# Kernel tuning notes

Measured on AMD Instinct MI355X. Metric: run time of the kernel, lower is better.

The kernel has to match this reference:

```python
import jax, jax.numpy as jnp
import numpy as np
from jax import lax

EPS_NORM = 1e-12   # F.normalize default eps
KS = 3             # fixed 3x3 window
K2 = KS * KS
MIN_CONN, MAX_CONN = 1, 8
NUM_GROUPS = 16    # largest divisor <=16 of C=128
GN_EPS = 1e-5


def _unfold3x3_reflect(x):
    # x: [B,C,H,W] -> patches [B,C,9,H,W] (reflect-padded 3x3 neighborhoods)
    B, C, H, W = x.shape
    p = jnp.pad(x, ((0, 0), (0, 0), (1, 1), (1, 1)), mode='reflect')
    pats = [p[:, :, dy:dy + H, dx:dx + W] for dy in range(KS) for dx in range(KS)]
    return jnp.stack(pats, axis=2)


def _df_counts(x):
    # DFDetector: mean over C, fixed Laplacian conv (zero pad), abs, per-batch min-max norm
    B = x.shape[0]
    avg = jnp.mean(x, axis=1, keepdims=True)  # [B,1,H,W]
    kern = jnp.array([[0., -1., 0.], [-1., 4., -1.], [0., -1., 0.]],
                     dtype=x.dtype).reshape(1, 1, 3, 3)
    df = jnp.abs(lax.conv_general_dilated(
        avg, kern, window_strides=(1, 1), padding=((1, 1), (1, 1)),
        dimension_numbers=('NCHW', 'OIHW', 'NCHW')))
    dmin = df.reshape(B, -1).min(axis=1).reshape(B, 1, 1, 1)
    dmax = df.reshape(B, -1).max(axis=1).reshape(B, 1, 1, 1)
    dn = (df - dmin) / (dmax - dmin + 1e-8)
    return MIN_CONN + jnp.round(dn * (MAX_CONN - MIN_CONN))  # [B,1,H,W], values in [1,8]


def _group_norm(x, w, b):
    B, C, H, W = x.shape
    g = x.reshape(B, NUM_GROUPS, -1)
    mu = g.mean(-1, keepdims=True)
    var = g.var(-1, keepdims=True)  # biased, matches torch GroupNorm
    g = (g - mu) * lax.rsqrt(var + GN_EPS)
    return g.reshape(B, C, H, W) * w[None, :, None, None] + b[None, :, None, None]


def setup_inputs() -> dict:
    key = jax.random.key(0)
    ks = jax.random.split(key, 7)
    B, C, H, W = 8, 128, 96, 96
    return {
        'x': jax.random.normal(ks[0], (B, C, H, W), jnp.float32),
        'gn_weight': jax.random.uniform(ks[1], (C,), jnp.float32, 0.5, 1.5),
        'gn_bias': jax.random.normal(ks[2], (C,), jnp.float32) * 0.1,
        'w1': jax.random.normal(ks[3], (2 * C, C), jnp.float32) * 0.02,
        'b1': jax.random.normal(ks[4], (2 * C,), jnp.float32) * 0.02,
        'w2': jax.random.normal(ks[5], (C, 2 * C), jnp.float32) * 0.02,
        'b2': jax.random.normal(ks[6], (C,), jnp.float32) * 0.02,
    }


def reference(x, gn_weight, gn_bias, w1, b1, w2, b2):
    B, C, H, W = x.shape
    P = H * W
    # per-pixel connection counts (integer k in [1,8]); non-differentiable in original
    counts = lax.stop_gradient(_df_counts(x))
    kvals = jnp.minimum(counts, K2).astype(jnp.int32).reshape(B, 1, P)

    patches = _unfold3x3_reflect(x).reshape(B, C, K2, P)
    xc = x.reshape(B, C, P)
    # L2 normalize over channel dim (F.normalize, eps=1e-12)
    cn = xc / jnp.maximum(jnp.linalg.norm(xc, axis=1, keepdims=True), EPS_NORM)
    pn = patches / jnp.maximum(jnp.linalg.norm(patches, axis=1, keepdims=True), EPS_NORM)

    sim = jnp.einsum('bcp,bckp->bkp', cn, pn)          # [B,9,P] cosine sims
    order = jnp.argsort(-sim, axis=1)                   # descending (== topk order)
    top_sim = jnp.take_along_axis(sim, order, axis=1)
    mask = jnp.arange(K2)[None, :, None] < kvals        # rank < k -> selected
    wts = jnp.exp(top_sim) * mask
    wts = wts / jnp.sum(wts, axis=1, keepdims=True)     # softmax over selected sims

    pat_sorted = jnp.take_along_axis(patches, order[:, None, :, :], axis=2)
    out = jnp.einsum('bckp,bkp->bcp', pat_sorted, wts).reshape(B, C, H, W)

    enhanced = out + _group_norm(x, gn_weight, gn_bias)
    h = jax.nn.relu(jnp.einsum('oi,bihw->bohw', w1, enhanced) + b1[None, :, None, None])
    ffn = jnp.einsum('oi,bihw->bohw', w2, h) + b2[None, :, None, None]
    return enhanced + ffn
```

## Files before the change

### kernel.cpp

```cpp
#include <hip/hip_runtime.h>

#define BD 8
#define CD 128
#define HD 96
#define WD 96
#define PD 9216
#define ND 73728

typedef __attribute__((ext_vector_type(8))) short short8;
typedef __attribute__((ext_vector_type(4))) float f32x4;

__device__ inline float bfu2f(unsigned int u) { return __uint_as_float(u << 16); }
__device__ inline unsigned short f2bfu(float f) {
  unsigned int u = __float_as_uint(f);
  u += 0x7fffu + ((u >> 16) & 1u);
  return (unsigned short)(u >> 16);
}

template<bool F32>
__device__ __forceinline__ float ldv(const void* __restrict__ p, size_t i) {
  if constexpr (F32) return ((const float*)p)[i];
  else return bfu2f(((const unsigned short*)p)[i]);
}

__global__ void k_init(unsigned long long* dmm, int* cnt) {
  int t = threadIdx.x;
  if (t < 8) dmm[t] = 0x7FEFFFFFFFFFFFFFULL;
  else if (t < 16) dmm[t] = 0ULL;
  if (t == 16) { cnt[0] = 0; cnt[1] = 0; }
}

__global__ void k_detect(const unsigned int* __restrict__ xw, int* __restrict__ cnt) {
  int t = blockIdx.x * 256 + threadIdx.x;
  uint4 w = ((const uint4*)xw)[t];
  int lz = (int)((w.x & 0xFFFFu) == 0u) + (int)((w.y & 0xFFFFu) == 0u) +
           (int)((w.z & 0xFFFFu) == 0u) + (int)((w.w & 0xFFFFu) == 0u);
  int e2 = (int)(((w.x >> 7) & 0xFFu) == 0xFFu) + (int)(((w.y >> 7) & 0xFFu) == 0xFFu) +
           (int)(((w.z >> 7) & 0xFFu) == 0xFFu) + (int)(((w.w >> 7) & 0xFFu) == 0xFFu);
  #pragma unroll
  for (int off = 32; off; off >>= 1) {
    lz += __shfl_down(lz, off);
    e2 += __shfl_down(e2, off);
  }
  if ((threadIdx.x & 63) == 0) { atomicAdd(&cnt[0], lz); atomicAdd(&cnt[1], e2); }
}

__global__ void k_flag(const int* __restrict__ cnt, int* __restrict__ flag) {
  *flag = (cnt[0] > 4096 || cnt[1] > 0) ? 1 : 0;
}

__global__ void k_cvtw(const void* __restrict__ w1, const void* __restrict__ w2,
                       unsigned short* __restrict__ wc, const int* __restrict__ flag) {
  bool f32 = (*flag != 0);
  int t = blockIdx.x * 256 + threadIdx.x;
  if (t < 32768)
    wc[t] = f32 ? f2bfu(((const float*)w1)[t]) : ((const unsigned short*)w1)[t];
  else {
    int u = t - 32768;
    wc[t] = f32 ? f2bfu(((const float*)w2)[u]) : ((const unsigned short*)w2)[u];
  }
}

__global__ void k_cvtb(const void* __restrict__ gw, const void* __restrict__ gb,
                       const void* __restrict__ b1, const void* __restrict__ b2,
                       float* __restrict__ prm, const int* __restrict__ flag) {
  bool f32 = (*flag != 0);
  int t = threadIdx.x;
  for (int i = t; i < 640; i += 256) {
    float v;
    if (i < 128)      v = f32 ? ((const float*)gw)[i]       : bfu2f(((const unsigned short*)gw)[i]);
    else if (i < 256) v = f32 ? ((const float*)gb)[i - 128] : bfu2f(((const unsigned short*)gb)[i - 128]);
    else if (i < 512) v = f32 ? ((const float*)b1)[i - 256] : bfu2f(((const unsigned short*)b1)[i - 256]);
    else              v = f32 ? ((const float*)b2)[i - 512] : bfu2f(((const unsigned short*)b2)[i - 512]);
    prm[i] = v;
  }
}

template<bool F32>
__device__ __forceinline__ void pmt_body(const void* __restrict__ x,
                                         float* __restrict__ xpm,
                                         double* __restrict__ avg, double* __restrict__ nrm,
                                         double* __restrict__ nrm2,
                                         double* __restrict__ gpart,
                                         float (*tile)[132], int lb) {
  const int t = threadIdx.x, px = t & 63, ci = t >> 6;
  const int gp0 = lb * 64, b = gp0 / PD, p0 = gp0 - b * PD;
  double sg[4] = {0.0, 0.0, 0.0, 0.0}, qg[4] = {0.0, 0.0, 0.0, 0.0};
  for (int j = 0; j < 32; ++j) {
    int c = ci * 32 + j;
    float v = ldv<F32>(x, (size_t)(b * CD + c) * PD + p0 + px);
    tile[px][c] = v;
    sg[j >> 3] += (double)v;
    qg[j >> 3] += (double)v * (double)v;
  }
  #pragma unroll
  for (int g = 0; g < 4; ++g) {
    #pragma unroll
    for (int off = 32; off; off >>= 1) {
      sg[g] += __shfl_down(sg[g], off);
      qg[g] += __shfl_down(qg[g], off);
    }
  }
  if (px == 0) {
    double* gp_ = gpart + (size_t)lb * 32;
    #pragma unroll
    for (int g = 0; g < 4; ++g) {
      gp_[(ci * 4 + g) * 2 + 0] = sg[g];
      gp_[(ci * 4 + g) * 2 + 1] = qg[g];
    }
  }
  __syncthreads();
  for (int i = t; i < 2048; i += 256) {
    int r = i >> 5, seg = i & 31;
    *(float4*)(xpm + (size_t)(gp0 + r) * 128 + seg * 4) = *(const float4*)&tile[r][seg * 4];
  }
  if (t < 64) {
    double s = 0.0, q = 0.0;
    for (int c = 0; c < 128; ++c) {
      float v = tile[t][c];
      s += (double)v;
      q += (double)v * (double)v;
    }
    double qq[4] = {0.0, 0.0, 0.0, 0.0};
    #pragma unroll
    for (int g = 0; g < 4; ++g)
      for (int i = 0; i < 32; ++i) {
        float v = tile[t][g * 32 + i];
        qq[g] += (double)v * (double)v;
      }
    avg[gp0 + t] = s * (1.0 / 128.0);
    nrm[gp0 + t] = sqrt(q);
    nrm2[gp0 + t] = ((qq[0] + qq[1]) + qq[2]) + qq[3];
  }
}
__global__ __launch_bounds__(256) void k_pmt(const void* __restrict__ x,
                                             const int* __restrict__ flag,
                                             float* __restrict__ xpm,
                                             double* __restrict__ avg,
                                             double* __restrict__ nrm,
                                             double* __restrict__ nrm2,
                                             double* __restrict__ gpart) {
  __shared__ float tile[64][132];
  const int lb = (blockIdx.x & 7) * 144 + (blockIdx.x >> 3);
  if (*flag) pmt_body<true>(x, xpm, avg, nrm, nrm2, gpart, tile, lb);
  else pmt_body<false>(x, xpm, avg, nrm, nrm2, gpart, tile, lb);
}

__global__ void k_gn2(const double* __restrict__ gpart, float* __restrict__ gn) {
  const int bg = blockIdx.x;
  const int b = bg >> 4, g = bg & 15;
  const int t = threadIdx.x;
  double s = 0.0, q = 0.0;
  for (int i = t; i < 144; i += 64) {
    const double* pp = gpart + (size_t)(b * 144 + i) * 32 + g * 2;
    s += pp[0];
    q += pp[1];
  }
  #pragma unroll
  for (int off = 32; off; off >>= 1) {
    s += __shfl_down(s, off);
    q += __shfl_down(q, off);
  }
  if (t == 0) {
    double mu = s / 73728.0;
    double var = q / 73728.0 - mu * mu;
    gn[bg] = (float)mu;
    gn[128 + bg] = (float)(1.0 / sqrt(var + 1e-5));
  }
}

__device__ inline double lap_df(const double* __restrict__ a, int b, int y, int x) {
  const double* ab = a + (size_t)b * PD;
  double v = 4.0 * ab[y * WD + x];
  if (y > 0)      v -= ab[(y - 1) * WD + x];
  if (y < HD - 1) v -= ab[(y + 1) * WD + x];
  if (x > 0)      v -= ab[y * WD + x - 1];
  if (x < WD - 1) v -= ab[y * WD + x + 1];
  return fabs(v);
}

__global__ void k_minmax(const double* __restrict__ avg, unsigned long long* __restrict__ dmm,
                         double* __restrict__ dfb) {
  __shared__ double mnW[4], mxW[4];
  int t = threadIdx.x;
  const int lb = (blockIdx.x & 7) * 36 + (blockIdx.x >> 3);
  int gp = lb * 256 + t;
  int b = gp / PD, p = gp - b * PD;
  double df = lap_df(avg, b, p / WD, p % WD);
  dfb[gp] = df;
  double mn = df, mx = df;
  #pragma unroll
  for (int off = 32; off; off >>= 1) {
    mn = fmin(mn, __shfl_down(mn, off));
    mx = fmax(mx, __shfl_down(mx, off));
  }
  if ((t & 63) == 0) { mnW[t >> 6] = mn; mxW[t >> 6] = mx; }
  __syncthreads();
  if (t == 0) {
    mn = fmin(fmin(mnW[0], mnW[1]), fmin(mnW[2], mnW[3]));
    mx = fmax(fmax(mxW[0], mxW[1]), fmax(mxW[2], mxW[3]));
    atomicMin(&dmm[b], (unsigned long long)__double_as_longlong(mn));
    atomicMax(&dmm[b + 8], (unsigned long long)__double_as_longlong(mx));
  }
}

__global__ __launch_bounds__(256, 3) void k_ipg(const float* __restrict__ xpm,
                                                const double* __restrict__ nrm,
                                                const double* __restrict__ nrm2,
                                                const double* __restrict__ dfb,
                                                const unsigned long long* __restrict__ dmm,
                                                const float* __restrict__ gn,
                                                const float* __restrict__ prm,
                                                unsigned short* __restrict__ eg) {
  __shared__ float tileF[12800];
  __shared__ double nsl[100];
  __shared__ double nsl2[64];
  float4* tile4 = (float4*)tileF;
  const float* gwf = prm;
  const float* gbf = prm + 128;

  const int t = threadIdx.x;
  const int lb = (blockIdx.x & 7) * 144 + (blockIdx.x >> 3);
  const int b = lb / 144;
  const int tid = lb - b * 144;
  const int ty = tid / 12, tx = tid - ty * 12;
  const int y0 = ty * 8, x0 = tx * 8;

  {
    const int s = t & 31, hpb = t >> 5;
    #pragma unroll
    for (int it = 0; it < 13; ++it) {
      int hp = it * 8 + hpb;
      if (hp < 100) {
        int hr = hp / 10, hc = hp - hr * 10;
        int gy = y0 - 1 + hr; gy = gy < 0 ? -gy : (gy >= HD ? 2 * HD - 2 - gy : gy);
        int gx = x0 - 1 + hc; gx = gx < 0 ? -gx : (gx >= WD ? 2 * WD - 2 - gx : gx);
        const float4* src = (const float4*)(xpm + (size_t)(b * PD + gy * WD + gx) * 128) + s;
        tile4[(hp * 32 + s) ^ (hp & 7)] = *src;
      }
    }
    if (t < 100) {
      int hr = t / 10, hc = t - hr * 10;
      int gy = y0 - 1 + hr; gy = gy < 0 ? -gy : (gy >= HD ? 2 * HD - 2 - gy : gy);
      int gx = x0 - 1 + hc; gx = gx < 0 ? -gx : (gx >= WD ? 2 * WD - 2 - gx : gx);
      nsl[t] = nrm[b * PD + gy * WD + gx];
    } else if (t >= 128 && t < 192) {
      int a2 = t - 128;
      nsl2[a2] = nrm2[b * PD + (y0 + (a2 >> 3)) * WD + x0 + (a2 & 7)];
    }
  }
  __syncthreads();

  const int a = t >> 2, q = t & 3;
  const int yl = a >> 3, xl = a & 7;
  const int y = y0 + yl, xx = x0 + xl;
  const int p = y * WD + xx;
  const int cpix = (yl + 1) * 10 + (xl + 1);
  const int cub = cpix * 32 + q * 8, csw = cpix & 7;

  double sd[9];
  {
    float cv[32];
    #pragma unroll
    for (int j4 = 0; j4 < 8; ++j4)
      *(float4*)(cv + 4 * j4) = tile4[(cub + j4) ^ csw];
    #pragma unroll
    for (int k = 0; k < 9; ++k) {
      if (k == 4) continue;
      int dy = k / 3, dx = k - dy * 3;
      int pix = (yl + dy) * 10 + (xl + dx);
      int ub = pix * 32 + q * 8, sw = pix & 7;
      double acc = 0.0;
      #pragma unroll
      for (int seg = 0; seg < 8; ++seg) {
        float4 nv = tile4[(ub + seg) ^ sw];
        acc += (double)cv[seg * 4 + 0] * (double)nv.x;
        acc += (double)cv[seg * 4 + 1] * (double)nv.y;
        acc += (double)cv[seg * 4 + 2] * (double)nv.z;
        acc += (double)cv[seg * 4 + 3] * (double)nv.w;
      }
      double v1 = __shfl_down(acc, 1);
      double v2 = __shfl_down(acc, 2);
      double v3 = __shfl_down(acc, 3);
      sd[k] = ((acc + v1) + v2) + v3;
    }
  }

  float wv[9];
  #pragma unroll
  for (int j = 0; j < 9; ++j) wv[j] = 0.f;
  if (q == 0) {
    double dmin = __longlong_as_double((long long)dmm[b]);
    double dmax = __longlong_as_double((long long)dmm[b + 8]);
    double df = dfb[b * PD + p];
    double dn = (df - dmin) / (dmax - dmin + 1e-8);
    int kk = 1 + (int)rint(dn * 7.0);
    kk = kk < 1 ? 1 : (kk > 8 ? 8 : kk);

    sd[4] = nsl2[a];
    double np_ = fmax(nsl[cpix], 1e-12);
    #pragma unroll
    for (int k = 0; k < 9; ++k) {
      int dy = k / 3, dx = k - dy * 3;
      double nq = fmax(nsl[(yl + dy) * 10 + (xl + dx)], 1e-12);
      sd[k] = sd[k] / (np_ * nq);
    }
    float w[9];
    float wsum = 0.f;
    #pragma unroll
    for (int j = 0; j < 9; ++j) {
      int rank = 0;
      #pragma unroll
      for (int i = 0; i < 9; ++i)
        rank += (sd[i] > sd[j]) || (sd[i] == sd[j] && i < j);
      w[j] = (rank < kk) ? expf((float)sd[j]) : 0.f;
      wsum += w[j];
    }
    float inv = 1.f / wsum;
    #pragma unroll
    for (int j = 0; j < 9; ++j) wv[j] = w[j] * inv;
  }
  #pragma unroll
  for (int j = 0; j < 9; ++j) wv[j] = __shfl(wv[j], (t & 63) & ~3);

  {
    float og[32];
    #pragma unroll
    for (int j = 0; j < 32; ++j) og[j] = 0.f;
    #pragma unroll
    for (int k = 0; k < 9; ++k) {
      int dy = k / 3, dx = k - dy * 3;
      int pix = (yl + dy) * 10 + (xl + dx);
      int ub = pix * 32 + q * 8, sw = pix & 7;
      #pragma unroll
      for (int seg = 0; seg < 8; ++seg) {
        float4 nv = tile4[(ub + seg) ^ sw];
        og[seg * 4 + 0] += wv[k] * nv.x;
        og[seg * 4 + 1] += wv[k] * nv.y;
        og[seg * 4 + 2] += wv[k] * nv.z;
        og[seg * 4 + 3] += wv[k] * nv.w;
      }
    }
    const int g16 = b * 16;
    unsigned short* egr = eg + (size_t)(b * PD + p) * 128 + q * 32;
    #pragma unroll
    for (int seg = 0; seg < 4; ++seg) {
      float4 cA = tile4[(cub + seg * 2) ^ csw];
      float4 cB = tile4[(cub + seg * 2 + 1) ^ csw];
      float cvv[8] = {cA.x, cA.y, cA.z, cA.w, cB.x, cB.y, cB.z, cB.w};
      int g = q * 4 + seg;
      float mu = gn[g16 + g], rs = gn[128 + g16 + g];
      unsigned int pkd[4];
      #pragma unroll
      for (int j = 0; j < 8; ++j) {
        int c = q * 32 + seg * 8 + j;
        float e = og[seg * 8 + j] + (cvv[j] - mu) * rs * gwf[c] + gbf[c];
        unsigned int h = (unsigned int)f2bfu(e);
        if (j & 1) pkd[j >> 1] |= h << 16;
        else pkd[j >> 1] = h;
      }
      uint4 v; v.x = pkd[0]; v.y = pkd[1]; v.z = pkd[2]; v.w = pkd[3];
      *(uint4*)(egr + seg * 8) = v;
    }
  }
}

__global__ __launch_bounds__(256, 3) void k_ffn(const unsigned short* __restrict__ eg,
                                                const float* __restrict__ prm,
                                                const unsigned short* __restrict__ wc,
                                                float* __restrict__ outp) {
  __shared__ unsigned short et[64][136];
  __shared__ unsigned short Hl[64][264];
  const float* b1f = prm + 256;
  const float* b2f = prm + 512;

  const int t = threadIdx.x;
  const int lb = (blockIdx.x & 7) * 144 + (blockIdx.x >> 3);
  const int gp0 = lb * 64;
  const int b = gp0 / PD, p0b = gp0 - b * PD;

  const unsigned short* wc1 = wc;
  const unsigned short* wc2 = wc + 32768;
  const int lane = t & 63, wave = t >> 6;
  const int r16 = lane & 15, quad = lane >> 4;

  {
    const uint4* eg4 = (const uint4*)(eg + (size_t)gp0 * 128);
    #pragma unroll
    for (int it = 0; it < 4; ++it) {
      int lin = it * 256 + t;
      int row = lin >> 4, c8 = lin & 15;
      *(uint4*)&et[row][c8 * 8] = eg4[lin];
    }
  }
  short8 wb1[16];
  #pragma unroll
  for (int kk = 0; kk < 4; ++kk)
    #pragma unroll
    for (int nt = 0; nt < 4; ++nt)
      wb1[kk * 4 + nt] = *(const short8*)(wc1 + (size_t)(wave * 64 + nt * 16 + r16) * 128 + kk * 32 + quad * 8);
  __syncthreads();

  f32x4 acc[16];
  #pragma unroll
  for (int i = 0; i < 16; ++i) acc[i] = (f32x4){0.f, 0.f, 0.f, 0.f};
  #pragma unroll
  for (int kk = 0; kk < 4; ++kk) {
    short8 afm[4];
    #pragma unroll
    for (int m = 0; m < 4; ++m)
      afm[m] = *(const short8*)&et[m * 16 + r16][kk * 32 + quad * 8];
    #pragma unroll
    for (int nt = 0; nt < 4; ++nt)
      #pragma unroll
      for (int m = 0; m < 4; ++m)
        acc[m * 4 + nt] = __builtin_amdgcn_mfma_f32_16x16x32_bf16(afm[m], wb1[kk * 4 + nt], acc[m * 4 + nt], 0, 0, 0);
  }
  #pragma unroll
  for (int nt = 0; nt < 4; ++nt) {
    int n = wave * 64 + nt * 16 + r16;
    float bias = b1f[n];
    #pragma unroll
    for (int m = 0; m < 4; ++m)
      #pragma unroll
      for (int r = 0; r < 4; ++r)
        Hl[m * 16 + quad * 4 + r][n] = f2bfu(fmaxf(acc[m * 4 + nt][r] + bias, 0.f));
  }
  short8 wb2[16];
  #pragma unroll
  for (int kk = 0; kk < 8; ++kk)
    #pragma unroll
    for (int nt = 0; nt < 2; ++nt)
      wb2[kk * 2 + nt] = *(const short8*)(wc2 + (size_t)(wave * 32 + nt * 16 + r16) * 256 + kk * 32 + quad * 8);
  __syncthreads();

  f32x4 acc2[8];
  #pragma unroll
  for (int i = 0; i < 8; ++i) acc2[i] = (f32x4){0.f, 0.f, 0.f, 0.f};
  #pragma unroll
  for (int kk = 0; kk < 8; ++kk) {
    short8 afm[4];
    #pragma unroll
    for (int m = 0; m < 4; ++m)
      afm[m] = *(const short8*)&Hl[m * 16 + r16][kk * 32 + quad * 8];
    #pragma unroll
    for (int nt = 0; nt < 2; ++nt)
      #pragma unroll
      for (int m = 0; m < 4; ++m)
        acc2[m * 2 + nt] = __builtin_amdgcn_mfma_f32_16x16x32_bf16(afm[m], wb2[kk * 2 + nt], acc2[m * 2 + nt], 0, 0, 0);
  }
  #pragma unroll
  for (int nt = 0; nt < 2; ++nt) {
    int n = wave * 32 + nt * 16 + r16;
    float bias = b2f[n];
    #pragma unroll
    for (int m = 0; m < 4; ++m) {
      int mloc0 = m * 16 + quad * 4;
      float4 o;
      o.x = acc2[m * 2 + nt][0] + bias + bfu2f(et[mloc0 + 0][n]);
      o.y = acc2[m * 2 + nt][1] + bias + bfu2f(et[mloc0 + 1][n]);
      o.z = acc2[m * 2 + nt][2] + bias + bfu2f(et[mloc0 + 2][n]);
      o.w = acc2[m * 2 + nt][3] + bias + bfu2f(et[mloc0 + 3][n]);
      *(float4*)(outp + (size_t)(b * CD + n) * PD + p0b + mloc0) = o;
    }
  }
}

extern "C" void kernel_launch(void* const* d_in, const int* in_sizes, int n_in,
                              void* d_out, int out_size, void* d_ws, size_t ws_size,
                              hipStream_t stream) {
  const void* x  = d_in[0];
  const void* gw = d_in[1];
  const void* gb = d_in[2];
  const void* w1 = d_in[3];
  const void* b1 = d_in[4];
  const void* w2 = d_in[5];
  const void* b2 = d_in[6];
  float* out = (float*)d_out;

  char* ws = (char*)d_ws;
  int* flag = (int*)ws;
  int* cnt = (int*)(ws + 16);
  unsigned long long* dmm = (unsigned long long*)(ws + 128);
  float* gn = (float*)(ws + 256);
  float* prm = (float*)(ws + 1280);
  unsigned short* wc = (unsigned short*)(ws + 3840);
  double* avg = (double*)(ws + 134912);
  double* nrm = (double*)(ws + 724736);
  double* nrm2 = (double*)(ws + 1314560);
  double* gpart = (double*)(ws + 1904384);
  double* dfb = (double*)(ws + 2199296);
  unsigned short* eg = (unsigned short*)(ws + 2789120);
  float* xpm = (float*)(ws + 21663488);

  k_init<<<1, 64, 0, stream>>>(dmm, cnt);
  k_detect<<<64, 256, 0, stream>>>((const unsigned int*)x, cnt);
  k_flag<<<1, 1, 0, stream>>>(cnt, flag);
  k_cvtw<<<256, 256, 0, stream>>>(w1, w2, wc, flag);
  k_cvtb<<<1, 256, 0, stream>>>(gw, gb, b1, b2, prm, flag);
  k_pmt<<<ND / 64, 256, 0, stream>>>(x, flag, xpm, avg, nrm, nrm2, gpart);
  k_gn2<<<128, 64, 0, stream>>>(gpart, gn);
  k_minmax<<<ND / 256, 256, 0, stream>>>(avg, dmm, dfb);
  k_ipg<<<ND / 64, 256, 0, stream>>>(xpm, nrm, nrm2, dfb, dmm, gn, prm, eg);
  k_ffn<<<ND / 64, 256, 0, stream>>>(eg, prm, wc, out);
}
```

Baseline: 188.3 us.

## Drop pixel-major transpose buffer and merge small setup kernels

The stats pass no longer writes a transposed pixel-major copy of x. It reads x directly in NCHW with coalesced per-pixel threads and computes the norms and group partial sums in registers. The gather kernel now loads the halo tile straight from the NCHW input with strided per-channel loads. The init, flag, weight and bias conversion kernels are fused into one launch, and group-norm finalisation is merged with the Laplacian min/max kernel, cutting the launch count from ten to six. This removes a full write and reread of the transposed activation copy, but the gather's scalar strided loads from x may be less efficient than the earlier float4 row reads.

```diff
diff --git a/kernel.cpp b/kernel.cpp
--- a/kernel.cpp
+++ b/kernel.cpp
@@ -23,16 +23,10 @@
   else return bfu2f(((const unsigned short*)p)[i]);
 }
 
-__global__ void k_init(unsigned long long* dmm, int* cnt) {
-  int t = threadIdx.x;
-  if (t < 8) dmm[t] = 0x7FEFFFFFFFFFFFFFULL;
-  else if (t < 16) dmm[t] = 0ULL;
-  if (t == 16) { cnt[0] = 0; cnt[1] = 0; }
-}
-
-__global__ void k_detect(const unsigned int* __restrict__ xw, int* __restrict__ cnt) {
-  int t = blockIdx.x * 256 + threadIdx.x;
-  uint4 w = ((const uint4*)xw)[t];
+__global__ void k_detect(const unsigned int* __restrict__ xw, int* __restrict__ dcnt) {
+  __shared__ int wl[4], we[4];
+  const int t = threadIdx.x;
+  uint4 w = ((const uint4*)xw)[blockIdx.x * 256 + t];
   int lz = (int)((w.x & 0xFFFFu) == 0u) + (int)((w.y & 0xFFFFu) == 0u) +
            (int)((w.z & 0xFFFFu) == 0u) + (int)((w.w & 0xFFFFu) == 0u);
   int e2 = (int)(((w.x >> 7) & 0xFFu) == 0xFFu) + (int)(((w.y >> 7) & 0xFFu) == 0xFFu) +
@@ -42,131 +36,105 @@
     lz += __shfl_down(lz, off);
     e2 += __shfl_down(e2, off);
   }
-  if ((threadIdx.x & 63) == 0) { atomicAdd(&cnt[0], lz); atomicAdd(&cnt[1], e2); }
-}
-
-__global__ void k_flag(const int* __restrict__ cnt, int* __restrict__ flag) {
-  *flag = (cnt[0] > 4096 || cnt[1] > 0) ? 1 : 0;
-}
-
-__global__ void k_cvtw(const void* __restrict__ w1, const void* __restrict__ w2,
-                       unsigned short* __restrict__ wc, const int* __restrict__ flag) {
-  bool f32 = (*flag != 0);
-  int t = blockIdx.x * 256 + threadIdx.x;
-  if (t < 32768)
-    wc[t] = f32 ? f2bfu(((const float*)w1)[t]) : ((const unsigned short*)w1)[t];
-  else {
-    int u = t - 32768;
-    wc[t] = f32 ? f2bfu(((const float*)w2)[u]) : ((const unsigned short*)w2)[u];
-  }
-}
-
-__global__ void k_cvtb(const void* __restrict__ gw, const void* __restrict__ gb,
-                       const void* __restrict__ b1, const void* __restrict__ b2,
-                       float* __restrict__ prm, const int* __restrict__ flag) {
-  bool f32 = (*flag != 0);
-  int t = threadIdx.x;
-  for (int i = t; i < 640; i += 256) {
-    float v;
-    if (i < 128)      v = f32 ? ((const float*)gw)[i]       : bfu2f(((const unsigned short*)gw)[i]);
-    else if (i < 256) v = f32 ? ((const float*)gb)[i - 128] : bfu2f(((const unsigned short*)gb)[i - 128]);
-    else if (i < 512) v = f32 ? ((const float*)b1)[i - 256] : bfu2f(((const unsigned short*)b1)[i - 256]);
-    else              v = f32 ? ((const float*)b2)[i - 512] : bfu2f(((const unsigned short*)b2)[i - 512]);
-    prm[i] = v;
+  if ((t & 63) == 0) { wl[t >> 6] = lz; we[t >> 6] = e2; }
+  __syncthreads();
+  if (t == 0) {
+    dcnt[blockIdx.x] = wl[0] + wl[1] + wl[2] + wl[3];
+    dcnt[64 + blockIdx.x] = we[0] + we[1] + we[2] + we[3];
+  }
+}
+
+__global__ void k_cvt(const void* __restrict__ w1, const void* __restrict__ w2,
+                      const void* __restrict__ gw, const void* __restrict__ gb,
+                      const void* __restrict__ b1, const void* __restrict__ b2,
+                      const int* __restrict__ dcnt,
+                      unsigned short* __restrict__ wc, float* __restrict__ prm,
+                      int* __restrict__ flag, unsigned long long* __restrict__ dmm) {
+  __shared__ int sflag;
+  const int t = threadIdx.x;
+  if (t < 64) {
+    int lz = dcnt[t], e2 = dcnt[64 + t];
+    #pragma unroll
+    for (int off = 32; off; off >>= 1) {
+      lz += __shfl_down(lz, off);
+      e2 += __shfl_down(e2, off);
+    }
+    if (t == 0) sflag = (lz > 4096 || e2 > 0) ? 1 : 0;
+  }
+  __syncthreads();
+  const bool f32 = sflag != 0;
+  const int blk = blockIdx.x;
+  if (blk < 256) {
+    int i = blk * 256 + t;
+    if (i < 32768)
+      wc[i] = f32 ? f2bfu(((const float*)w1)[i]) : ((const unsigned short*)w1)[i];
+    else {
+      int u = i - 32768;
+      wc[i] = f32 ? f2bfu(((const float*)w2)[u]) : ((const unsigned short*)w2)[u];
+    }
+  } else {
+    for (int i = t; i < 640; i += 256) {
+      float v;
+      if (i < 128)      v = f32 ? ((const float*)gw)[i]       : bfu2f(((const unsigned short*)gw)[i]);
+      else if (i < 256) v = f32 ? ((const float*)gb)[i - 128] : bfu2f(((const unsigned short*)gb)[i - 128]);
+      else if (i < 512) v = f32 ? ((const float*)b1)[i - 256] : bfu2f(((const unsigned short*)b1)[i - 256]);
+      else              v = f32 ? ((const float*)b2)[i - 512] : bfu2f(((const unsigned short*)b2)[i - 512]);
+      prm[i] = v;
+    }
+    if (t < 8) dmm[t] = 0x7FEFFFFFFFFFFFFFULL;
+    else if (t < 16) dmm[t - 8 + 8] = 0ULL;
+    if (t == 16) *flag = sflag;
   }
 }
 
 template<bool F32>
-__device__ __forceinline__ void pmt_body(const void* __restrict__ x,
-                                         float* __restrict__ xpm,
-                                         double* __restrict__ avg, double* __restrict__ nrm,
-                                         double* __restrict__ nrm2,
-                                         double* __restrict__ gpart,
-                                         float (*tile)[132], int lb) {
-  const int t = threadIdx.x, px = t & 63, ci = t >> 6;
-  const int gp0 = lb * 64, b = gp0 / PD, p0 = gp0 - b * PD;
-  double sg[4] = {0.0, 0.0, 0.0, 0.0}, qg[4] = {0.0, 0.0, 0.0, 0.0};
-  for (int j = 0; j < 32; ++j) {
-    int c = ci * 32 + j;
-    float v = ldv<F32>(x, (size_t)(b * CD + c) * PD + p0 + px);
-    tile[px][c] = v;
-    sg[j >> 3] += (double)v;
-    qg[j >> 3] += (double)v * (double)v;
-  }
-  #pragma unroll
-  for (int g = 0; g < 4; ++g) {
+__device__ __forceinline__ void stats_body(const void* __restrict__ x,
+                                           double* __restrict__ avg, double* __restrict__ nrm,
+                                           double* __restrict__ nrm2, double* __restrict__ gpart,
+                                           int lb) {
+  const int t = threadIdx.x;
+  const int gp0 = lb * 256;
+  const int b = gp0 / PD, p0 = gp0 - b * PD;
+  const size_t base = (size_t)b * CD * PD + p0 + t;
+  double s = 0.0, q = 0.0;
+  double qq0 = 0.0, qq1 = 0.0, qq2 = 0.0, qq3 = 0.0;
+  double* gslot = gpart + (size_t)(lb * 4 + (t >> 6)) * 32;
+  #pragma unroll
+  for (int g = 0; g < 16; ++g) {
+    double gs = 0.0, gq = 0.0;
+    #pragma unroll
+    for (int j = 0; j < 8; ++j) {
+      const int c = g * 8 + j;
+      double dv = (double)ldv<F32>(x, base + (size_t)c * PD);
+      s += dv;
+      q += dv * dv;
+      if (g < 4) qq0 += dv * dv;
+      else if (g < 8) qq1 += dv * dv;
+      else if (g < 12) qq2 += dv * dv;
+      else qq3 += dv * dv;
+      gs += dv;
+      gq += dv * dv;
+    }
     #pragma unroll
     for (int off = 32; off; off >>= 1) {
-      sg[g] += __shfl_down(sg[g], off);
-      qg[g] += __shfl_down(qg[g], off);
-    }
-  }
-  if (px == 0) {
-    double* gp_ = gpart + (size_t)lb * 32;
-    #pragma unroll
-    for (int g = 0; g < 4; ++g) {
-      gp_[(ci * 4 + g) * 2 + 0] = sg[g];
-      gp_[(ci * 4 + g) * 2 + 1] = qg[g];
-    }
-  }
-  __syncthreads();
-  for (int i = t; i < 2048; i += 256) {
-    int r = i >> 5, seg = i & 31;
-    *(float4*)(xpm + (size_t)(gp0 + r) * 128 + seg * 4) = *(const float4*)&tile[r][seg * 4];
-  }
-  if (t < 64) {
-    double s = 0.0, q = 0.0;
-    for (int c = 0; c < 128; ++c) {
-      float v = tile[t][c];
-      s += (double)v;
-      q += (double)v * (double)v;
-    }
-    double qq[4] = {0.0, 0.0, 0.0, 0.0};
-    #pragma unroll
-    for (int g = 0; g < 4; ++g)
-      for (int i = 0; i < 32; ++i) {
-        float v = tile[t][g * 32 + i];
-        qq[g] += (double)v * (double)v;
-      }
-    avg[gp0 + t] = s * (1.0 / 128.0);
-    nrm[gp0 + t] = sqrt(q);
-    nrm2[gp0 + t] = ((qq[0] + qq[1]) + qq[2]) + qq[3];
-  }
-}
-__global__ __launch_bounds__(256) void k_pmt(const void* __restrict__ x,
-                                             const int* __restrict__ flag,
-                                             float* __restrict__ xpm,
-                                             double* __restrict__ avg,
-                                             double* __restrict__ nrm,
-                                             double* __restrict__ nrm2,
-                                             double* __restrict__ gpart) {
-  __shared__ float tile[64][132];
-  const int lb = (blockIdx.x & 7) * 144 + (blockIdx.x >> 3);
-  if (*flag) pmt_body<true>(x, xpm, avg, nrm, nrm2, gpart, tile, lb);
-  else pmt_body<false>(x, xpm, avg, nrm, nrm2, gpart, tile, lb);
-}
-
-__global__ void k_gn2(const double* __restrict__ gpart, float* __restrict__ gn) {
-  const int bg = blockIdx.x;
-  const int b = bg >> 4, g = bg & 15;
-  const int t = threadIdx.x;
-  double s = 0.0, q = 0.0;
-  for (int i = t; i < 144; i += 64) {
-    const double* pp = gpart + (size_t)(b * 144 + i) * 32 + g * 2;
-    s += pp[0];
-    q += pp[1];
-  }
-  #pragma unroll
-  for (int off = 32; off; off >>= 1) {
-    s += __shfl_down(s, off);
-    q += __shfl_down(q, off);
-  }
-  if (t == 0) {
-    double mu = s / 73728.0;
-    double var = q / 73728.0 - mu * mu;
-    gn[bg] = (float)mu;
-    gn[128 + bg] = (float)(1.0 / sqrt(var + 1e-5));
-  }
+      gs += __shfl_down(gs, off);
+      gq += __shfl_down(gq, off);
+    }
+    if ((t & 63) == 0) { gslot[g * 2] = gs; gslot[g * 2 + 1] = gq; }
+  }
+  avg[gp0 + t] = s * (1.0 / 128.0);
+  nrm[gp0 + t] = sqrt(q);
+  nrm2[gp0 + t] = ((qq0 + qq1) + qq2) + qq3;
+}
+__global__ __launch_bounds__(256) void k_stats(const void* __restrict__ x,
+                                               const int* __restrict__ flag,
+                                               double* __restrict__ avg,
+                                               double* __restrict__ nrm,
+                                               double* __restrict__ nrm2,
+                                               double* __restrict__ gpart) {
+  const int lb = (blockIdx.x & 7) * 36 + (blockIdx.x >> 3);
+  if (*flag) stats_body<true>(x, avg, nrm, nrm2, gpart, lb);
+  else stats_body<false>(x, avg, nrm, nrm2, gpart, lb);
 }
 
 __device__ inline double lap_df(const double* __restrict__ a, int b, int y, int x) {
@@ -179,42 +147,69 @@
   return fabs(v);
 }
 
-__global__ void k_minmax(const double* __restrict__ avg, unsigned long long* __restrict__ dmm,
-                         double* __restrict__ dfb) {
-  __shared__ double mnW[4], mxW[4];
-  int t = threadIdx.x;
-  const int lb = (blockIdx.x & 7) * 36 + (blockIdx.x >> 3);
-  int gp = lb * 256 + t;
-  int b = gp / PD, p = gp - b * PD;
-  double df = lap_df(avg, b, p / WD, p % WD);
-  dfb[gp] = df;
-  double mn = df, mx = df;
-  #pragma unroll
-  for (int off = 32; off; off >>= 1) {
-    mn = fmin(mn, __shfl_down(mn, off));
-    mx = fmax(mx, __shfl_down(mx, off));
-  }
-  if ((t & 63) == 0) { mnW[t >> 6] = mn; mxW[t >> 6] = mx; }
-  __syncthreads();
-  if (t == 0) {
-    mn = fmin(fmin(mnW[0], mnW[1]), fmin(mnW[2], mnW[3]));
-    mx = fmax(fmax(mxW[0], mxW[1]), fmax(mxW[2], mxW[3]));
-    atomicMin(&dmm[b], (unsigned long long)__double_as_longlong(mn));
-    atomicMax(&dmm[b + 8], (unsigned long long)__double_as_longlong(mx));
-  }
-}
-
-__global__ __launch_bounds__(256, 3) void k_ipg(const float* __restrict__ xpm,
-                                                const double* __restrict__ nrm,
-                                                const double* __restrict__ nrm2,
-                                                const double* __restrict__ dfb,
-                                                const unsigned long long* __restrict__ dmm,
-                                                const float* __restrict__ gn,
-                                                const float* __restrict__ prm,
-                                                unsigned short* __restrict__ eg) {
-  __shared__ float tileF[12800];
-  __shared__ double nsl[100];
-  __shared__ double nsl2[64];
+__global__ void k_mg(const double* __restrict__ avg, unsigned long long* __restrict__ dmm,
+                     double* __restrict__ dfb, const double* __restrict__ gpart,
+                     float* __restrict__ gn) {
+  __shared__ double red[8];
+  const int t = threadIdx.x;
+  if (blockIdx.x < 288) {
+    const int lb = ((int)blockIdx.x & 7) * 36 + ((int)blockIdx.x >> 3);
+    int gp = lb * 256 + t;
+    int b = gp / PD, p = gp - b * PD;
+    double df = lap_df(avg, b, p / WD, p % WD);
+    dfb[gp] = df;
+    double mn = df, mx = df;
+    #pragma unroll
+    for (int off = 32; off; off >>= 1) {
+      mn = fmin(mn, __shfl_down(mn, off));
+      mx = fmax(mx, __shfl_down(mx, off));
+    }
+    if ((t & 63) == 0) { red[t >> 6] = mn; red[4 + (t >> 6)] = mx; }
+    __syncthreads();
+    if (t == 0) {
+      mn = fmin(fmin(red[0], red[1]), fmin(red[2], red[3]));
+      mx = fmax(fmax(red[4], red[5]), fmax(red[6], red[7]));
+      atomicMin(&dmm[b], (unsigned long long)__double_as_longlong(mn));
+      atomicMax(&dmm[b + 8], (unsigned long long)__double_as_longlong(mx));
+    }
+  } else {
+    const int bg = blockIdx.x - 288;
+    const int b = bg >> 4, g = bg & 15;
+    double s = 0.0, q = 0.0;
+    if (t < 144) {
+      const double* pp = gpart + (size_t)(b * 144 + t) * 32 + g * 2;
+      s = pp[0];
+      q = pp[1];
+    }
+    #pragma unroll
+    for (int off = 32; off; off >>= 1) {
+      s += __shfl_down(s, off);
+      q += __shfl_down(q, off);
+    }
+    if ((t & 63) == 0) { red[t >> 6] = s; red[4 + (t >> 6)] = q; }
+    __syncthreads();
+    if (t == 0) {
+      double S = ((red[0] + red[1]) + red[2]) + red[3];
+      double Q = ((red[4] + red[5]) + red[6]) + red[7];
+      double mu = S / 73728.0;
+      double var = Q / 73728.0 - mu * mu;
+      gn[bg] = (float)mu;
+      gn[128 + bg] = (float)(1.0 / sqrt(var + 1e-5));
+    }
+  }
+}
+
+template<bool F32>
+__device__ __forceinline__ void ipg_body(const void* __restrict__ x,
+                                         const double* __restrict__ nrm,
+                                         const double* __restrict__ nrm2,
+                                         const double* __restrict__ dfb,
+                                         const unsigned long long* __restrict__ dmm,
+                                         const float* __restrict__ gn,
+                                         const float* __restrict__ prm,
+                                         unsigned short* __restrict__ eg,
+                                         float* __restrict__ tileF,
+                                         double* __restrict__ nsl, double* __restrict__ nsl2) {
   float4* tile4 = (float4*)tileF;
   const float* gwf = prm;
   const float* gbf = prm + 128;
@@ -227,24 +222,27 @@
   const int y0 = ty * 8, x0 = tx * 8;
 
   {
-    const int s = t & 31, hpb = t >> 5;
-    #pragma unroll
-    for (int it = 0; it < 13; ++it) {
-      int hp = it * 8 + hpb;
-      if (hp < 100) {
-        int hr = hp / 10, hc = hp - hr * 10;
-        int gy = y0 - 1 + hr; gy = gy < 0 ? -gy : (gy >= HD ? 2 * HD - 2 - gy : gy);
-        int gx = x0 - 1 + hc; gx = gx < 0 ? -gx : (gx >= WD ? 2 * WD - 2 - gx : gx);
-        const float4* src = (const float4*)(xpm + (size_t)(b * PD + gy * WD + gx) * 128) + s;
-        tile4[(hp * 32 + s) ^ (hp & 7)] = *src;
-      }
-    }
-    if (t < 100) {
-      int hr = t / 10, hc = t - hr * 10;
+    const int hp = t & 127;
+    if (hp < 100) {
+      int hr = hp / 10, hc = hp - hr * 10;
       int gy = y0 - 1 + hr; gy = gy < 0 ? -gy : (gy >= HD ? 2 * HD - 2 - gy : gy);
       int gx = x0 - 1 + hc; gx = gx < 0 ? -gx : (gx >= WD ? 2 * WD - 2 - gx : gx);
-      nsl[t] = nrm[b * PD + gy * WD + gx];
-    } else if (t >= 128 && t < 192) {
+      const size_t pbase = (size_t)b * CD * PD + (size_t)gy * WD + gx;
+      const int sw = hp & 7;
+      #pragma unroll
+      for (int it = 0; it < 16; ++it) {
+        int s = it * 2 + (t >> 7);
+        size_t cb = pbase + (size_t)(4 * s) * PD;
+        float4 v;
+        v.x = ldv<F32>(x, cb);
+        v.y = ldv<F32>(x, cb + PD);
+        v.z = ldv<F32>(x, cb + 2 * PD);
+        v.w = ldv<F32>(x, cb + 3 * PD);
+        tile4[(hp * 32 + s) ^ sw] = v;
+      }
+      if (t < 100) nsl[t] = nrm[b * PD + gy * WD + gx];
+    }
+    if (t >= 128 && t < 192) {
       int a2 = t - 128;
       nsl2[a2] = nrm2[b * PD + (y0 + (a2 >> 3)) * WD + x0 + (a2 & 7)];
     }
@@ -364,6 +362,21 @@
     }
   }
 }
+__global__ __launch_bounds__(256, 3) void k_ipg(const void* __restrict__ x,
+                                                const int* __restrict__ flag,
+                                                const double* __restrict__ nrm,
+                                                const double* __restrict__ nrm2,
+                                                const double* __restrict__ dfb,
+                                                const unsigned long long* __restrict__ dmm,
+                                                const float* __restrict__ gn,
+                                                const float* __restrict__ prm,
+                                                unsigned short* __restrict__ eg) {
+  __shared__ float tileF[12800];
+  __shared__ double nsl[100];
+  __shared__ double nsl2[64];
+  if (*flag) ipg_body<true>(x, nrm, nrm2, dfb, dmm, gn, prm, eg, tileF, nsl, nsl2);
+  else ipg_body<false>(x, nrm, nrm2, dfb, dmm, gn, prm, eg, tileF, nsl, nsl2);
+}
 
 __global__ __launch_bounds__(256, 3) void k_ffn(const unsigned short* __restrict__ eg,
                                                 const float* __restrict__ prm,
@@ -480,27 +493,22 @@
 
   char* ws = (char*)d_ws;
   int* flag = (int*)ws;
-  int* cnt = (int*)(ws + 16);
-  unsigned long long* dmm = (unsigned long long*)(ws + 128);
-  float* gn = (float*)(ws + 256);
-  float* prm = (float*)(ws + 1280);
-  unsigned short* wc = (unsigned short*)(ws + 3840);
-  double* avg = (double*)(ws + 134912);
-  double* nrm = (double*)(ws + 724736);
-  double* nrm2 = (double*)(ws + 1314560);
-  double* gpart = (double*)(ws + 1904384);
-  double* dfb = (double*)(ws + 2199296);
-  unsigned short* eg = (unsigned short*)(ws + 2789120);
-  float* xpm = (float*)(ws + 21663488);
-
-  k_init<<<1, 64, 0, stream>>>(dmm, cnt);
-  k_detect<<<64, 256, 0, stream>>>((const unsigned int*)x, cnt);
-  k_flag<<<1, 1, 0, stream>>>(cnt, flag);
-  k_cvtw<<<256, 256, 0, stream>>>(w1, w2, wc, flag);
-  k_cvtb<<<1, 256, 0, stream>>>(gw, gb, b1, b2, prm, flag);
-  k_pmt<<<ND / 64, 256, 0, stream>>>(x, flag, xpm, avg, nrm, nrm2, gpart);
-  k_gn2<<<128, 64, 0, stream>>>(gpart, gn);
-  k_minmax<<<ND / 256, 256, 0, stream>>>(avg, dmm, dfb);
-  k_ipg<<<ND / 64, 256, 0, stream>>>(xpm, nrm, nrm2, dfb, dmm, gn, prm, eg);
+  int* dcnt = (int*)(ws + 16);
+  unsigned long long* dmm = (unsigned long long*)(ws + 640);
+  float* gn = (float*)(ws + 768);
+  float* prm = (float*)(ws + 1792);
+  unsigned short* wc = (unsigned short*)(ws + 4352);
+  double* avg = (double*)(ws + 135424);
+  double* nrm = (double*)(ws + 725248);
+  double* nrm2 = (double*)(ws + 1315072);
+  double* gpart = (double*)(ws + 1904896);
+  double* dfb = (double*)(ws + 2199808);
+  unsigned short* eg = (unsigned short*)(ws + 2789632);
+
+  k_detect<<<64, 256, 0, stream>>>((const unsigned int*)x, dcnt);
+  k_cvt<<<257, 256, 0, stream>>>(w1, w2, gw, gb, b1, b2, dcnt, wc, prm, flag, dmm);
+  k_stats<<<288, 256, 0, stream>>>(x, flag, avg, nrm, nrm2, gpart);
+  k_mg<<<416, 256, 0, stream>>>(avg, dmm, dfb, gpart, gn);
+  k_ipg<<<ND / 64, 256, 0, stream>>>(x, flag, nrm, nrm2, dfb, dmm, gn, prm, eg);
   k_ffn<<<ND / 64, 256, 0, stream>>>(eg, prm, wc, out);
 }
```

Result: slower. 210.6 us (+11.9%).
